# Optimization experiments

Hardware: AMD Instinct MI355X
Metric: run time of the kernel (lower is better)

The kernel has to match this reference:

```python
import jax, jax.numpy as jnp
import numpy as np
import math

INPUT_SIZE = 4096
PTS_PER_EPOCH = 100


def _grid_bounds(input_size):
    # Replicates get_grid(): n_row = n_col = ceil(sqrt(input_size)),
    # each cell is the central half of its grid square (gap = size/4 on each side).
    n = math.ceil(math.sqrt(input_size))
    size = 1.0 / n
    gap = size / 4.0
    i = jnp.arange(input_size)
    gy = i // n  # row index (uses n_row == n_col)
    gx = i % n
    x_low = gx.astype(jnp.float32) * size + gap
    y_low = gy.astype(jnp.float32) * size + gap
    x_high = x_low + 2.0 * gap
    y_high = y_low + 2.0 * gap
    return x_low, x_high, y_low, y_high


def setup_inputs() -> dict:
    key = jax.random.key(0)
    k1, k2, k3 = jax.random.split(key, 3)
    batch = 8192
    n_fibers = 64
    total_pts = 10000  # 100 * max_epoch
    inp = jax.random.normal(k1, (batch, INPUT_SIZE), dtype=jnp.float32)
    fibers_x = jax.random.uniform(k2, (n_fibers, total_pts), dtype=jnp.float32)
    fibers_y = jax.random.uniform(k3, (n_fibers, total_pts), dtype=jnp.float32)
    return {"input": inp, "fibers_x": fibers_x, "fibers_y": fibers_y, "current_epoch": 7}


def reference(input, fibers_x, fibers_y, current_epoch):
    t = current_epoch * PTS_PER_EPOCH
    # points of all fibers for this epoch, flattened: (P,) with P = n_fibers*100
    px = fibers_x[:, t:t + PTS_PER_EPOCH].reshape(-1)
    py = fibers_y[:, t:t + PTS_PER_EPOCH].reshape(-1)
    x_low, x_high, y_low, y_high = _grid_bounds(INPUT_SIZE)
    # broadcast point-in-rectangle test: (P, 1) vs (N,) -> (P, N)
    in_cell = ((x_low[None, :] <= px[:, None]) & (px[:, None] <= x_high[None, :]) &
               (y_low[None, :] <= py[:, None]) & (py[:, None] <= y_high[None, :]))
    touching = jnp.any(in_cell, axis=0)  # (N,)
    mask = jnp.where(touching, 0.0, 1.0).astype(input.dtype)
    return input * mask[None, :]
```

## Files before the change

### kernel.cpp

```cpp
#include <hip/hip_runtime.h>


#define N_COLS 4096
#define PTS_PER_EPOCH 100
#define N_GRID 64
#define TOTAL_PTS 10000
#define N_FIBERS 64
#define BLOCK 256
#define GRID_BLOCKS 2048
#define STRIDE (GRID_BLOCKS * BLOCK)
#define ITER 16
#define PF 8

typedef float f32x4 __attribute__((ext_vector_type(4)));

__global__ __launch_bounds__(BLOCK) void fused_fbm_dropout(
    const float* __restrict__ fx,
    const float* __restrict__ fy,
    const int* __restrict__ epoch_p,
    const f32x4* __restrict__ in4,
    f32x4* __restrict__ out4,
    int n4) {
    __shared__ float mask[N_COLS];
    const int tid = threadIdx.x;
    const int i0 = blockIdx.x * BLOCK + tid;
    const bool fast = (n4 == GRID_BLOCKS * BLOCK * ITER);

    f32x4 a[PF];
    if (fast) {
#pragma unroll
        for (int k = 0; k < PF; ++k) a[k] = in4[i0 + k * STRIDE];
    }

    for (int i = tid; i < N_COLS; i += BLOCK) mask[i] = 1.0f;
    __syncthreads();

    const int t = epoch_p[0] * PTS_PER_EPOCH;
    for (int g = tid; g < (N_FIBERS * PTS_PER_EPOCH) / 4; g += BLOCK) {
        const int f  = g / 25;
        const int j4 = g - f * 25;
        const int base4 = (f * TOTAL_PTS + t) / 4 + j4;
        const f32x4 px4 = ((const f32x4*)fx)[base4];
        const f32x4 py4 = ((const f32x4*)fy)[base4];
#pragma unroll
        for (int k = 0; k < 4; ++k) {
            const float ux = px4[k] * 64.0f;
            const float uy = py4[k] * 64.0f;
            const float gxf = floorf(ux);
            const float gyf = floorf(uy);
            const float frx = ux - gxf;
            const float fry = uy - gyf;
            if (frx >= 0.25f && frx <= 0.75f && fry >= 0.25f && fry <= 0.75f) {
                const int gx = (int)gxf;
                const int gy = (int)gyf;
                if (gx >= 0 && gx < N_GRID && gy >= 0 && gy < N_GRID) {
                    mask[gy * N_GRID + gx] = 0.0f;
                }
            }
        }
    }
    __syncthreads();

    const f32x4 m = ((const f32x4*)mask)[i0 & (N_COLS / 4 - 1)];

    if (fast) {
#pragma unroll
        for (int k = 0; k < ITER; ++k) {
            const f32x4 v = a[k & (PF - 1)] * m;
            if (k + PF < ITER)
                a[k & (PF - 1)] = in4[i0 + (k + PF) * STRIDE];
            out4[i0 + k * STRIDE] = v;
        }
    } else {
        for (int i = i0; i < n4; i += STRIDE) {
            out4[i] = in4[i] * m;
        }
    }
}

extern "C" void kernel_launch(void* const* d_in, const int* in_sizes, int n_in,
                              void* d_out, int out_size, void* d_ws, size_t ws_size,
                              hipStream_t stream) {
    const float* inp   = (const float*)d_in[0];
    const float* fx    = (const float*)d_in[1];
    const float* fy    = (const float*)d_in[2];
    const int*   epoch = (const int*)d_in[3];

    const int n4 = out_size / 4;
    fused_fbm_dropout<<<GRID_BLOCKS, BLOCK, 0, stream>>>(
        fx, fy, epoch, (const f32x4*)inp, (f32x4*)d_out, n4);
}
```

Measured before the change: 249.2 us.

## Split mask build into separate single-block kernel and stream apply kernel

Unfuses the mask construction from the elementwise multiply: a single 1024-thread block builds the 4096-entry mask in global workspace, then a second kernel applies it with each thread handling four quarter-strided vectors. This removes the redundant per-block mask rebuild (2048 blocks each recomputing 6400 points plus barriers) from the bandwidth-bound pass. It adds a second kernel launch with a serial dependency, and drops the explicit register prefetch in favor of more blocks with four loads each.

```diff
diff --git a/kernel.cpp b/kernel.cpp
--- a/kernel.cpp
+++ b/kernel.cpp
@@ -6,37 +6,20 @@
 #define N_GRID 64
 #define TOTAL_PTS 10000
 #define N_FIBERS 64
-#define BLOCK 256
-#define GRID_BLOCKS 2048
-#define STRIDE (GRID_BLOCKS * BLOCK)
-#define ITER 16
-#define PF 8
 
 typedef float f32x4 __attribute__((ext_vector_type(4)));
 
-__global__ __launch_bounds__(BLOCK) void fused_fbm_dropout(
+__global__ __launch_bounds__(1024) void build_mask_kernel(
     const float* __restrict__ fx,
     const float* __restrict__ fy,
     const int* __restrict__ epoch_p,
-    const f32x4* __restrict__ in4,
-    f32x4* __restrict__ out4,
-    int n4) {
-    __shared__ float mask[N_COLS];
+    float* __restrict__ mask) {
     const int tid = threadIdx.x;
-    const int i0 = blockIdx.x * BLOCK + tid;
-    const bool fast = (n4 == GRID_BLOCKS * BLOCK * ITER);
-
-    f32x4 a[PF];
-    if (fast) {
-#pragma unroll
-        for (int k = 0; k < PF; ++k) a[k] = in4[i0 + k * STRIDE];
-    }
-
-    for (int i = tid; i < N_COLS; i += BLOCK) mask[i] = 1.0f;
+    ((f32x4*)mask)[tid] = (f32x4){1.0f, 1.0f, 1.0f, 1.0f};
     __syncthreads();
 
     const int t = epoch_p[0] * PTS_PER_EPOCH;
-    for (int g = tid; g < (N_FIBERS * PTS_PER_EPOCH) / 4; g += BLOCK) {
+    for (int g = tid; g < (N_FIBERS * PTS_PER_EPOCH) / 4; g += 1024) {
         const int f  = g / 25;
         const int j4 = g - f * 25;
         const int base4 = (f * TOTAL_PTS + t) / 4 + j4;
@@ -59,22 +42,31 @@
             }
         }
     }
-    __syncthreads();
+}
 
-    const f32x4 m = ((const f32x4*)mask)[i0 & (N_COLS / 4 - 1)];
+__global__ __launch_bounds__(256) void apply_mask_kernel(
+    const f32x4* __restrict__ in4,
+    const f32x4* __restrict__ mask4,
+    f32x4* __restrict__ out4,
+    int n4) {
+    const int i0 = blockIdx.x * 256 + threadIdx.x;
+    const int q = n4 >> 2;
 
-    if (fast) {
-#pragma unroll
-        for (int k = 0; k < ITER; ++k) {
-            const f32x4 v = a[k & (PF - 1)] * m;
-            if (k + PF < ITER)
-                a[k & (PF - 1)] = in4[i0 + (k + PF) * STRIDE];
-            out4[i0 + k * STRIDE] = v;
-        }
+    if (((q & (N_COLS / 4 - 1)) == 0) && (q << 2) == n4) {
+        if (i0 >= q) return;
+        const f32x4 m = mask4[i0 & (N_COLS / 4 - 1)];
+        const f32x4 a0 = in4[i0];
+        const f32x4 a1 = in4[i0 + q];
+        const f32x4 a2 = in4[i0 + 2 * q];
+        const f32x4 a3 = in4[i0 + 3 * q];
+        out4[i0]         = a0 * m;
+        out4[i0 + q]     = a1 * m;
+        out4[i0 + 2 * q] = a2 * m;
+        out4[i0 + 3 * q] = a3 * m;
     } else {
-        for (int i = i0; i < n4; i += STRIDE) {
-            out4[i] = in4[i] * m;
-        }
+        const int stride = gridDim.x * 256;
+        for (int i = i0; i < n4; i += stride)
+            out4[i] = in4[i] * mask4[i & (N_COLS / 4 - 1)];
     }
 }
 
@@ -85,8 +77,13 @@
     const float* fx    = (const float*)d_in[1];
     const float* fy    = (const float*)d_in[2];
     const int*   epoch = (const int*)d_in[3];
+    float* mask = (float*)d_ws;
+
+    build_mask_kernel<<<1, 1024, 0, stream>>>(fx, fy, epoch, mask);
 
     const int n4 = out_size / 4;
-    fused_fbm_dropout<<<GRID_BLOCKS, BLOCK, 0, stream>>>(
-        fx, fy, epoch, (const f32x4*)inp, (f32x4*)d_out, n4);
+    const int q  = n4 >> 2;
+    const int grid = (q + 255) / 256;
+    apply_mask_kernel<<<grid, 256, 0, stream>>>(
+        (const f32x4*)inp, (const f32x4*)d_ws, (f32x4*)d_out, n4);
 }
```

Result: no change. 245.1 us (-1.6%).
